# Optimization experiments

Measured on AMD Instinct MI355X. Metric: run time of the kernel, lower is better.

## Reference

```python
import jax, jax.numpy as jnp
import numpy as np

SCALAR_DIM = 452          # 2 + 6 + (110+1)*4
GRID_C, GRID_H, GRID_W = 2, 32, 18
GRID_FLAT = GRID_C * GRID_H * GRID_W  # 1152
OBS_DIM = SCALAR_DIM + GRID_FLAT      # 1604
CNN_OUT, SC_OUT, HID, N_ACT = 128, 64, 128, 2305
CNN_FLAT = 64 * 8 * 5                 # 32x18 -> 16x9 -> 8x5
T, B = 256, 128


def setup_inputs() -> dict:
    key = jax.random.key(0)
    ks = jax.random.split(key, 24)
    p = lambda k, shape: jax.random.normal(k, shape, jnp.float32) * 0.02
    return dict(
        obs_seq=jax.random.uniform(ks[0], (T, B, OBS_DIM), jnp.float32),
        h0=jnp.zeros((1, B, HID), jnp.float32),
        c0=jnp.zeros((1, B, HID), jnp.float32),
        done_mask=jax.random.randint(ks[1], (T, B), 0, 2) > 0,
        conv1_w=p(ks[2], (32, GRID_C, 3, 3)), conv1_b=jnp.zeros((32,), jnp.float32),
        conv2_w=p(ks[3], (64, 32, 3, 3)),     conv2_b=jnp.zeros((64,), jnp.float32),
        conv3_w=p(ks[4], (64, 64, 3, 3)),     conv3_b=jnp.zeros((64,), jnp.float32),
        fc_w=p(ks[5], (CNN_OUT, CNN_FLAT)),   fc_b=jnp.zeros((CNN_OUT,), jnp.float32),
        s1_w=p(ks[6], (64, SCALAR_DIM)),      s1_b=jnp.zeros((64,), jnp.float32),
        s2_w=p(ks[7], (SC_OUT, 64)),          s2_b=jnp.zeros((SC_OUT,), jnp.float32),
        w_ih=p(ks[8], (4 * HID, CNN_OUT + SC_OUT)),
        w_hh=p(ks[9], (4 * HID, HID)),
        b_ih=jnp.zeros((4 * HID,), jnp.float32),
        b_hh=jnp.zeros((4 * HID,), jnp.float32),
        pol_w=p(ks[10], (N_ACT, HID)), pol_b=jnp.zeros((N_ACT,), jnp.float32),
        val_w=p(ks[11], (1, HID)),     val_b=jnp.zeros((1,), jnp.float32),
    )


def _conv(x, w, b, stride):
    y = jax.lax.conv_general_dilated(
        x, w, (stride, stride), ((1, 1), (1, 1)),
        dimension_numbers=("NCHW", "OIHW", "NCHW"))
    return y + b[None, :, None, None]


def reference(obs_seq, h0, c0, done_mask,
              conv1_w, conv1_b, conv2_w, conv2_b, conv3_w, conv3_b,
              fc_w, fc_b, s1_w, s1_b, s2_w, s2_b,
              w_ih, w_hh, b_ih, b_hh, pol_w, pol_b, val_w, val_b):
    Tt, Bb, _ = obs_seq.shape
    flat = obs_seq.reshape(Tt * Bb, -1)
    scalars = flat[:, :SCALAR_DIM]
    grid = flat[:, SCALAR_DIM:SCALAR_DIM + GRID_FLAT].reshape(-1, GRID_C, GRID_H, GRID_W)

    # CNN encoder
    x = jax.nn.relu(_conv(grid, conv1_w, conv1_b, 1))
    x = jax.nn.relu(_conv(x, conv2_w, conv2_b, 2))
    x = jax.nn.relu(_conv(x, conv3_w, conv3_b, 2))
    cnn = jax.nn.relu(x.reshape(x.shape[0], -1) @ fc_w.T + fc_b)

    # scalar MLP
    sc = jax.nn.relu(jax.nn.relu(scalars @ s1_w.T + s1_b) @ s2_w.T + s2_b)

    emb = jnp.concatenate([cnn, sc], axis=-1).reshape(Tt, Bb, -1)  # (T,B,192)

    # episode-reset mask applied BEFORE each step (for t>0, from done[t-1])
    keep = jnp.concatenate(
        [jnp.ones((1, Bb), jnp.float32),
         1.0 - done_mask[:-1].astype(jnp.float32)], axis=0)[..., None]  # (T,B,1)

    def step(carry, inp):
        h, c = carry
        x_t, k_t = inp
        h = h * k_t
        c = c * k_t
        g = x_t @ w_ih.T + h @ w_hh.T + b_ih + b_hh
        i, f, gg, o = jnp.split(g, 4, axis=-1)  # torch gate order i,f,g,o
        c = jax.nn.sigmoid(f) * c + jax.nn.sigmoid(i) * jnp.tanh(gg)
        h = jax.nn.sigmoid(o) * jnp.tanh(c)
        return (h, c), h

    (h_f, c_f), outs = jax.lax.scan(step, (h0[0], c0[0]), (emb, keep))

    logits = outs @ pol_w.T + pol_b   # (T,B,n_actions)
    values = outs @ val_w.T + val_b   # (T,B,1)
    return logits, values, h_f[None], c_f[None]
```

## Files before the change

kernel.cpp:

```cpp
#include <hip/hip_runtime.h>


typedef __attribute__((ext_vector_type(8))) short v8s;
typedef __attribute__((ext_vector_type(4))) float v4f;
typedef __attribute__((ext_vector_type(4))) unsigned int v4u;

#define DEV static __device__ __forceinline__

DEV unsigned int cvtpk(float lo, float hi){
  unsigned int d;
  asm("v_cvt_pk_bf16_f32 %0, %1, %2" : "=v"(d) : "v"(lo), "v"(hi));
  return d;
}
DEV unsigned short f2bf(float x){ return (unsigned short)(cvtpk(x, x) & 0xffffu); }
DEV float bf2f(unsigned short h){ return __uint_as_float(((unsigned int)h) << 16); }
DEV unsigned int pkbf(float a, float b){ return cvtpk(a, b); }
DEV v4f MFMA(v8s a, v8s b, v4f c){ return __builtin_amdgcn_mfma_f32_16x16x32_bf16(a, b, c, 0, 0, 0); }
DEV v4f vzero(){ v4f z = {0.f, 0.f, 0.f, 0.f}; return z; }
DEV float relu(float x){ return x > 0.f ? x : 0.f; }
DEV float sigm(float x){ return 1.0f / (1.0f + __expf(-x)); }
DEV float tanhfast(float x){
  x = fminf(15.0f, fmaxf(-15.0f, x));
  float e = __expf(2.0f * x);
  return (e - 1.0f) / (e + 1.0f);
}
DEV uint2 pack4(v4f a, float4 b){
  return make_uint2(cvtpk(relu(a[0]+b.x), relu(a[1]+b.y)),
                    cvtpk(relu(a[2]+b.z), relu(a[3]+b.w)));
}
union U8S { v4u u4; v8s s8; };

__global__ __launch_bounds__(256) void pack_all(
    const float* __restrict__ c1w, const float* __restrict__ c2w,
    const float* __restrict__ c3w, const float* __restrict__ fcw,
    const float* __restrict__ s1w, const float* __restrict__ s2w,
    const float* __restrict__ wih, const float* __restrict__ whh,
    const float* __restrict__ pw,
    unsigned short* __restrict__ w1p, unsigned short* __restrict__ w2p,
    unsigned short* __restrict__ w3p, unsigned short* __restrict__ fcp,
    unsigned short* __restrict__ s1p, unsigned short* __restrict__ s2p,
    unsigned short* __restrict__ lsp, unsigned short* __restrict__ pop){
  int b = blockIdx.x;
  const float *src, *src2 = nullptr; unsigned short* dst;
  int N, K, KS, CI, mode, rel;
  if      (b < 4)   { src=c1w; dst=w1p; N=32;  K=24;  KS=1;  CI=2;  mode=4; rel=b; }
  else if (b < 76)  { src=c2w; dst=w2p; N=64;  K=288; KS=9;  CI=32; mode=1; rel=b-4; }
  else if (b < 220) { src=c3w; dst=w3p; N=64;  K=576; KS=18; CI=64; mode=1; rel=b-76; }
  else if (b < 1500){ src=fcw; dst=fcp; N=128; K=2560;KS=80; CI=0;  mode=2; rel=b-220; }
  else if (b < 1620){ src=s1w; dst=s1p; N=64;  K=452; KS=15; CI=0;  mode=0; rel=b-1500; }
  else if (b < 1636){ src=s2w; dst=s2p; N=64;  K=64;  KS=2;  CI=0;  mode=0; rel=b-1620; }
  else if (b < 2276){ src=wih; src2=whh; dst=lsp; N=512; K=320; KS=10; CI=0; mode=3; rel=b-1636; }
  else              { src=pw;  dst=pop; N=2305;K=128; KS=4;  CI=0;  mode=0; rel=b-2276; }
  int idx = rel * 256 + threadIdx.x;
  int e  = idx & 7;
  int l  = (idx >> 3) & 63;
  int fs = idx >> 9;
  int ks = fs % KS;
  int nt = fs / KS;
  int n = nt * 16 + (l & 15);
  int k = ks * 32 + (l >> 4) * 8 + e;
  float v = 0.f;
  if (n < N && k < K){
    if (mode == 0)      v = src[n * K + k];
    else if (mode == 1){ int p9 = k / CI, ci = k - p9 * CI; v = src[(n * CI + ci) * 9 + p9]; }
    else if (mode == 2){ int pos = k >> 6, ci = k & 63;     v = src[n * 2560 + ci * 40 + pos]; }
    else if (mode == 3) v = (k < 192) ? src[n * 192 + k] : src2[n * 128 + (k - 192)];
    else { int dy = k >> 3, r = k & 7, dx = r >> 1, ci = r & 1;
           if (dx < 3) v = src[(n * 2 + ci) * 9 + dy * 3 + dx]; }
  }
  dst[idx] = f2bf(v);
}

__global__ __launch_bounds__(512) void bias_kernel(const float* __restrict__ bih,
    const float* __restrict__ bhh, float* __restrict__ bias512){
  int t = threadIdx.x;
  if (t < 512) bias512[t] = bih[t] + bhh[t];
}

__global__ __launch_bounds__(256) void mlp_kernel(const float* __restrict__ obs,
    const unsigned short* __restrict__ s1p, const unsigned short* __restrict__ s2p,
    const float* __restrict__ s1b, const float* __restrict__ s2b,
    unsigned short* __restrict__ emb){
  __shared__ __align__(16) unsigned short xl[32 * 488];
  __shared__ __align__(16) unsigned short h1[32 * 72];
  int tid = threadIdx.x, w = tid >> 6, l = tid & 63, i = l & 15, u = l >> 4;
  long s0 = (long)blockIdx.x * 32;
  for (int idx = tid; idx < 32 * 113; idx += 256){
    int r = idx / 113, q = idx - r * 113;
    float4 v = *(const float4*)&obs[(s0 + r) * 1604 + q * 4];
    *(uint2*)&xl[r * 488 + q * 4] = make_uint2(pkbf(v.x, v.y), pkbf(v.z, v.w));
  }
  for (int idx = tid; idx < 32 * 28; idx += 256){
    int r = idx / 28, k = 452 + (idx - r * 28);
    xl[r * 488 + k] = 0;
  }
  __syncthreads();
  v4f acc0 = vzero(), acc1 = vzero();
  const v8s* F1 = (const v8s*)s1p;
  #pragma unroll
  for (int ks = 0; ks < 15; ++ks){
    v8s bb = F1[(w * 15 + ks) * 64 + l];
    v8s aa0 = *(const v8s*)&xl[(0 * 16 + i) * 488 + ks * 32 + u * 8];
    v8s aa1 = *(const v8s*)&xl[(1 * 16 + i) * 488 + ks * 32 + u * 8];
    acc0 = MFMA(aa0, bb, acc0);
    acc1 = MFMA(aa1, bb, acc1);
  }
  float b1 = s1b[w * 16 + i];
  #pragma unroll
  for (int r = 0; r < 4; ++r){
    float v0 = relu(acc0[r] + b1);
    float v1 = relu(acc1[r] + b1);
    h1[(u * 4 + r) * 72 + w * 16 + i] = f2bf(v0);
    h1[(16 + u * 4 + r) * 72 + w * 16 + i] = f2bf(v1);
  }
  __syncthreads();
  v4f a20 = vzero(), a21 = vzero();
  const v8s* F2 = (const v8s*)s2p;
  #pragma unroll
  for (int ks = 0; ks < 2; ++ks){
    v8s bb = F2[(w * 2 + ks) * 64 + l];
    v8s aa0 = *(const v8s*)&h1[(0 * 16 + i) * 72 + ks * 32 + u * 8];
    v8s aa1 = *(const v8s*)&h1[(1 * 16 + i) * 72 + ks * 32 + u * 8];
    a20 = MFMA(aa0, bb, a20);
    a21 = MFMA(aa1, bb, a21);
  }
  float b2 = s2b[w * 16 + i];
  #pragma unroll
  for (int r = 0; r < 4; ++r){
    float v0 = relu(a20[r] + b2);
    float v1 = relu(a21[r] + b2);
    emb[(s0 + u * 4 + r) * 192 + 128 + w * 16 + i] = f2bf(v0);
    emb[(s0 + 16 + u * 4 + r) * 192 + 128 + w * 16 + i] = f2bf(v1);
  }
}

#define ACT1o 0
#define ACT2o 43520
#define GRIDo 68864
#define SWZ(p) ((((p) >> 1) & 7) << 4)

__global__ __launch_bounds__(512, 2) void conv_kernel(const float* __restrict__ obs,
    const unsigned short* __restrict__ w1p, const unsigned short* __restrict__ w2p,
    const unsigned short* __restrict__ w3p,
    const float* __restrict__ b1v, const float* __restrict__ b2v, const float* __restrict__ b3v,
    unsigned short* __restrict__ act3g){
  __shared__ __align__(16) char lds[74496];
  int tid = threadIdx.x, w = tid >> 6, l = tid & 63, i = l & 15, u = l >> 4;
  int ct = w & 3;
  int ph = w >> 2;
  const v8s* W1 = (const v8s*)w1p;
  const v8s* W2 = (const v8s*)w2p;
  const v8s* W3 = (const v8s*)w3p;
  v8s w1f0 = W1[l], w1f1 = W1[64 + l];
  float4 bc1a = *(const float4*)&b1v[u * 4];
  float4 bc1b = *(const float4*)&b1v[16 + u * 4];
  float4 bc2  = *(const float4*)&b2v[ct * 16 + u * 4];
  float4 bc3  = *(const float4*)&b3v[ct * 16 + u * 4];
  for (int idx = tid; idx < 18624; idx += 512) *(unsigned int*)(lds + idx * 4) = 0u;
  int soff[4];
  #pragma unroll
  for (int j = 0; j < 4; ++j){
    int p = tid * 4 + j, r = p / 18, c = p - r * 18;
    soff[j] = ((r + 1) * 20 + (c + 1)) * 4;
  }
  __syncthreads();
  long sbase = (long)blockIdx.x * 64;
  if (tid < 144){
    const float4* gp = (const float4*)(obs + sbase * 1604 + 452);
    float4 a = gp[tid], b = gp[tid + 144];
    *(unsigned int*)(lds + GRIDo + soff[0]) = pkbf(a.x, b.x);
    *(unsigned int*)(lds + GRIDo + soff[1]) = pkbf(a.y, b.y);
    *(unsigned int*)(lds + GRIDo + soff[2]) = pkbf(a.z, b.z);
    *(unsigned int*)(lds + GRIDo + soff[3]) = pkbf(a.w, b.w);
  }
  __syncthreads();

  int praw3 = ph * 16 + i;
  int oh3 = praw3 / 5, ow3 = praw3 - oh3 * 5;
  int pr3 = (2 * oh3) * 11 + 2 * ow3;
  int praw3s = 32 + i;
  int pos3s = praw3s > 39 ? 39 : praw3s;
  int oh3s = pos3s / 5, ow3s = pos3s - oh3s * 5;
  int pr3s = (2 * oh3s) * 11 + 2 * ow3s;
  bool small3 = (w < 4);

  for (int it = 0; it < 64; ++it){
    long s = sbase + it;
    int gbo = GRIDo + (it & 1) * 2816;
    int z2; asm("s_mov_b32 %0, 0" : "=s"(z2) : "s"(it));
    v8s w2f[9];
    #pragma unroll
    for (int t = 0; t < 9; ++t) w2f[t] = W2[(ct * 9 + t) * 64 + l + z2];
    float4 pa, pb; bool pf = (it < 63) && (tid < 144);
    if (pf){
      const float4* gp = (const float4*)(obs + (s + 1) * 1604 + 452);
      pa = gp[tid]; pb = gp[tid + 144];
    }
    #pragma unroll
    for (int k = 0; k < 5; ++k){
      int ntl = w + 8 * k;
      if (ntl < 36){
        int pos = ntl * 16 + i;
        int oh = pos / 18, ow = pos - oh * 18;
        int glin = gbo + ((oh + u) * 20 + ow) * 4;
        U8S gv;
        gv.u4.x = *(const unsigned int*)(lds + glin);
        gv.u4.y = *(const unsigned int*)(lds + glin + 4);
        gv.u4.z = *(const unsigned int*)(lds + glin + 8);
        gv.u4.w = *(const unsigned int*)(lds + glin + 12);
        v4f a0 = MFMA(w1f0, gv.s8, vzero());
        v4f a1 = MFMA(w1f1, gv.s8, vzero());
        int p1 = (oh + 1) * 20 + (ow + 1);
        int sA = SWZ(p1);
        *(uint2*)(lds + ACT1o + ((p1 * 64 + u * 8) ^ sA))      = pack4(a0, bc1a);
        *(uint2*)(lds + ACT1o + ((p1 * 64 + 32 + u * 8) ^ sA)) = pack4(a1, bc1b);
      }
    }
    __syncthreads();
    #pragma unroll
    for (int kk = 0; kk < 5; ++kk){
      int ntl = ph + 2 * kk;
      if (ntl < 9){
        int pos2 = ntl * 16 + i;
        int oh = pos2 / 9, ow = pos2 - oh * 9;
        int pr0 = (2 * oh) * 20 + 2 * ow;
        v4f a = vzero();
        #pragma unroll
        for (int dy = 0; dy < 3; ++dy)
          #pragma unroll
          for (int dx = 0; dx < 3; ++dx){
            int p = pr0 + dy * 20 + dx;
            int byte = (p * 64 + u * 16) ^ SWZ(p);
            v8s bf = *(const v8s*)(lds + ACT1o + byte);
            a = MFMA(w2f[dy * 3 + dx], bf, a);
          }
        int p2 = (oh + 1) * 11 + (ow + 1);
        *(uint2*)(lds + ACT2o + ((p2 * 128 + ct * 32 + u * 8) ^ SWZ(p2))) = pack4(a, bc2);
      }
    }
    if (pf){
      int gbn = GRIDo + ((it + 1) & 1) * 2816;
      *(unsigned int*)(lds + gbn + soff[0]) = pkbf(pa.x, pb.x);
      *(unsigned int*)(lds + gbn + soff[1]) = pkbf(pa.y, pb.y);
      *(unsigned int*)(lds + gbn + soff[2]) = pkbf(pa.z, pb.z);
      *(unsigned int*)(lds + gbn + soff[3]) = pkbf(pa.w, pb.w);
    }
    __syncthreads();
    {
      int z3; asm("s_mov_b32 %0, 0" : "=s"(z3) : "s"(it));
      v4f c3 = vzero(), c3s = vzero();
      #pragma unroll
      for (int ksh = 0; ksh < 2; ++ksh){
        v8s w3h[9];
        #pragma unroll
        for (int t = 0; t < 9; ++t) w3h[t] = W3[(ct * 18 + ksh * 9 + t) * 64 + l + z3];
        #pragma unroll
        for (int t = 0; t < 9; ++t){
          int ks = ksh * 9 + t, tap = ks >> 1, h = ks & 1;
          int dy = tap / 3, dx = tap - dy * 3;
          int dpp = dy * 11 + dx;
          {
            int p = pr3 + dpp;
            int byte = (p * 128 + h * 64 + u * 16) ^ SWZ(p);
            v8s bf = *(const v8s*)(lds + ACT2o + byte);
            c3 = MFMA(w3h[t], bf, c3);
          }
          if (small3){
            int p = pr3s + dpp;
            int byte = (p * 128 + h * 64 + u * 16) ^ SWZ(p);
            v8s bf = *(const v8s*)(lds + ACT2o + byte);
            c3s = MFMA(w3h[t], bf, c3s);
          }
        }
      }
      unsigned short* dg = act3g + s * 2560;
      *(uint2*)(dg + praw3 * 64 + ct * 16 + u * 4) = pack4(c3, bc3);
      if (small3 && praw3s < 40)
        *(uint2*)(dg + praw3s * 64 + ct * 16 + u * 4) = pack4(c3s, bc3);
    }
  }
}

__global__ __launch_bounds__(256) void fc_kernel(const unsigned short* __restrict__ act3g,
    const unsigned short* __restrict__ fcp, const float* __restrict__ fcb,
    unsigned short* __restrict__ emb){
  __shared__ __align__(16) unsigned short al[64 * 264];
  int tid = threadIdx.x, w = tid >> 6, l = tid & 63, i = l & 15, u = l >> 4;
  long s0 = (long)blockIdx.x * 64;
  v4f acc[4][2];
  #pragma unroll
  for (int mt = 0; mt < 4; ++mt){ acc[mt][0] = vzero(); acc[mt][1] = vzero(); }
  const v8s* F = (const v8s*)fcp;
  for (int kc = 0; kc < 10; ++kc){
    __syncthreads();
    for (int idx = tid; idx < 64 * 32; idx += 256){
      int r = idx >> 5, q = idx & 31;
      *(v8s*)&al[r * 264 + q * 8] = *(const v8s*)&act3g[(s0 + r) * 2560 + kc * 256 + q * 8];
    }
    __syncthreads();
    #pragma unroll
    for (int ksl = 0; ksl < 8; ++ksl){
      v8s b0 = F[((w * 2 + 0) * 80 + kc * 8 + ksl) * 64 + l];
      v8s b1 = F[((w * 2 + 1) * 80 + kc * 8 + ksl) * 64 + l];
      #pragma unroll
      for (int mt = 0; mt < 4; ++mt){
        v8s aa = *(const v8s*)&al[(mt * 16 + i) * 264 + ksl * 32 + u * 8];
        acc[mt][0] = MFMA(aa, b0, acc[mt][0]);
        acc[mt][1] = MFMA(aa, b1, acc[mt][1]);
      }
    }
  }
  float fb0 = fcb[(w * 2) * 16 + i], fb1 = fcb[(w * 2 + 1) * 16 + i];
  #pragma unroll
  for (int mt = 0; mt < 4; ++mt)
    #pragma unroll
    for (int r = 0; r < 4; ++r){
      float v0 = relu(acc[mt][0][r] + fb0);
      float v1 = relu(acc[mt][1][r] + fb1);
      emb[(s0 + mt * 16 + u * 4 + r) * 192 + (w * 2) * 16 + i] = f2bf(v0);
      emb[(s0 + mt * 16 + u * 4 + r) * 192 + (w * 2 + 1) * 16 + i] = f2bf(v1);
    }
}

__global__ __launch_bounds__(256) void segprep_kernel(const void* __restrict__ dmask,
    unsigned int* __restrict__ segs, int4* __restrict__ gtab, int* __restrict__ meta){
  __shared__ int cnt[257], off[257], place[257];
  __shared__ int notInt;
  int tid = threadIdx.x;
  for (int idx = tid; idx < 257; idx += 256){ cnt[idx] = 0; place[idx] = 0; }
  if (tid == 0) notInt = 0;
  __syncthreads();
  const unsigned char* p8 = (const unsigned char*)dmask;
  int nz = 0;
  for (int idx = tid; idx < 2048; idx += 256)
    if (p8[idx * 4 + 1] | p8[idx * 4 + 2] | p8[idx * 4 + 3]) nz = 1;
  if (nz) notInt = 1;
  __syncthreads();
  bool m32 = (notInt == 0);
  const int* p32 = (const int*)dmask;
  if (tid < 128){
    int b = tid, ts = 0;
    for (int t = 0; t < 256; ++t){
      bool d = (t == 255) ? true : (m32 ? (p32[t * 128 + b] != 0) : (p8[t * 128 + b] != 0));
      if (d){ atomicAdd(&cnt[t - ts + 1], 1); ts = t + 1; }
    }
  }
  __syncthreads();
  if (tid == 0){
    int acc = 0;
    for (int len = 1; len <= 256; ++len){ off[len] = acc; acc += cnt[len]; }
    int G = 0;
    for (int len = 1; len <= 256; ++len){
      int c = cnt[len], g = 0;
      while (c > 0){
        int take = c < 32 ? c : 32;
        gtab[G] = make_int4(len, off[len] + g * 32, take, 0);
        ++G; c -= 32; ++g;
      }
    }
    meta[0] = G;
  }
  __syncthreads();
  if (tid < 128){
    int b = tid, ts = 0;
    for (int t = 0; t < 256; ++t){
      bool d = (t == 255) ? true : (m32 ? (p32[t * 128 + b] != 0) : (p8[t * 128 + b] != 0));
      if (d){
        int len = t - ts + 1;
        int slot = off[len] + atomicAdd(&place[len], 1);
        segs[slot] = (unsigned int)(b | (ts << 8));
        ts = t + 1;
      }
    }
  }
}

__global__ __launch_bounds__(512) void lstm_kernel(
    const unsigned short* __restrict__ emb, const unsigned short* __restrict__ lstmp,
    const float* __restrict__ bias512,
    const float* __restrict__ h0, const float* __restrict__ c0,
    const unsigned int* __restrict__ segs, const int4* __restrict__ gtab,
    const int* __restrict__ meta,
    unsigned short* __restrict__ outsb, float* __restrict__ hf, float* __restrict__ cf){
  int grp = blockIdx.x;
  if (grp >= meta[0]) return;
  int4 gd = gtab[grp];
  int len = gd.x, base = gd.y, nseg = gd.z;
  __shared__ __align__(16) unsigned short hbuf[2][32 * 136];
  __shared__ int sb[32], st[32];
  int tid = threadIdx.x, w = tid >> 6, l = tid & 63, i = l & 15, u = l >> 4;
  if (tid < 32){
    unsigned int sv = segs[base + (tid < nseg ? tid : 0)];
    sb[tid] = (int)(sv & 127u);
    st[tid] = (int)((sv >> 8) & 255u);
  }
  __syncthreads();
  int j = w * 16 + i;
  float cst[2][4];
  #pragma unroll
  for (int mt = 0; mt < 2; ++mt)
    #pragma unroll
    for (int r = 0; r < 4; ++r){
      int slot = mt * 16 + u * 4 + r;
      float cv = 0.f, hv = 0.f;
      if (st[slot] == 0){ cv = c0[sb[slot] * 128 + j]; hv = h0[sb[slot] * 128 + j]; }
      cst[mt][r] = cv;
      hbuf[0][slot * 136 + j] = f2bf(hv);
    }
  float bi = bias512[j], bff = bias512[128 + j], bg = bias512[256 + j], bo = bias512[384 + j];
  int bA0 = sb[i], tA0 = st[i];
  int bA1 = sb[16 + i], tA1 = st[16 + i];
  __syncthreads();
  const v8s* LP = (const v8s*)lstmp;
  for (int step = 0; step < len; ++step){
    int pb = step & 1;
    v4f gi0 = vzero(), gi1 = vzero(), gf0 = vzero(), gf1 = vzero();
    v4f gg0 = vzero(), gg1 = vzero(), go0 = vzero(), go1 = vzero();
    #pragma unroll
    for (int ks = 0; ks < 10; ++ks){
      v8s a0, a1;
      if (ks < 6){
        a0 = *(const v8s*)&emb[((long)(tA0 + step) * 128 + bA0) * 192 + ks * 32 + u * 8];
        a1 = *(const v8s*)&emb[((long)(tA1 + step) * 128 + bA1) * 192 + ks * 32 + u * 8];
      } else {
        int koff = (ks - 6) * 32 + u * 8;
        a0 = *(const v8s*)&hbuf[pb][i * 136 + koff];
        a1 = *(const v8s*)&hbuf[pb][(16 + i) * 136 + koff];
      }
      v8s b_i = LP[((w) * 10 + ks) * 64 + l];
      v8s b_f = LP[((w + 8) * 10 + ks) * 64 + l];
      v8s b_g = LP[((w + 16) * 10 + ks) * 64 + l];
      v8s b_o = LP[((w + 24) * 10 + ks) * 64 + l];
      gi0 = MFMA(a0, b_i, gi0); gi1 = MFMA(a1, b_i, gi1);
      gf0 = MFMA(a0, b_f, gf0); gf1 = MFMA(a1, b_f, gf1);
      gg0 = MFMA(a0, b_g, gg0); gg1 = MFMA(a1, b_g, gg1);
      go0 = MFMA(a0, b_o, go0); go1 = MFMA(a1, b_o, go1);
    }
    #pragma unroll
    for (int mt = 0; mt < 2; ++mt)
      #pragma unroll
      for (int r = 0; r < 4; ++r){
        int slot = mt * 16 + u * 4 + r;
        float giv = mt ? gi1[r] : gi0[r];
        float gfv = mt ? gf1[r] : gf0[r];
        float ggv = mt ? gg1[r] : gg0[r];
        float gov = mt ? go1[r] : go0[r];
        float iv = sigm(giv + bi);
        float fv = sigm(gfv + bff);
        float gv = tanhfast(ggv + bg);
        float ov = sigm(gov + bo);
        float cv = fv * cst[mt][r] + iv * gv;
        cst[mt][r] = cv;
        float hv = ov * tanhfast(cv);
        unsigned short hb = f2bf(hv);
        hbuf[pb ^ 1][slot * 136 + j] = hb;
        if (slot < nseg){
          outsb[((long)(st[slot] + step) * 128 + sb[slot]) * 128 + j] = hb;
          if (st[slot] + len == 256 && step == len - 1){
            hf[sb[slot] * 128 + j] = hv;
            cf[sb[slot] * 128 + j] = cv;
          }
        }
      }
    __syncthreads();
  }
}

__global__ __launch_bounds__(256) void heads_kernel(const unsigned short* __restrict__ outsb,
    const unsigned short* __restrict__ polp, const float* __restrict__ polb,
    const float* __restrict__ vw, const float* __restrict__ vb,
    float* __restrict__ logits, float* __restrict__ values){
  __shared__ __align__(16) unsigned short al[64 * 136];
  int tid = threadIdx.x, w = tid >> 6, l = tid & 63, i = l & 15, u = l >> 4;
  long s0 = (long)blockIdx.x * 64;
  for (int idx = tid; idx < 64 * 16; idx += 256){
    int r = idx >> 4, q = idx & 15;
    *(v8s*)&al[r * 136 + q * 8] = *(const v8s*)&outsb[(s0 + r) * 128 + q * 8];
  }
  __syncthreads();
  v8s af[4][4];
  #pragma unroll
  for (int mt = 0; mt < 4; ++mt)
    #pragma unroll
    for (int ks = 0; ks < 4; ++ks)
      af[mt][ks] = *(const v8s*)&al[(mt * 16 + i) * 136 + ks * 32 + u * 8];
  const v8s* P = (const v8s*)polp;
  for (int nt = w; nt < 145; nt += 4){
    v4f acc[4];
    #pragma unroll
    for (int mt = 0; mt < 4; ++mt) acc[mt] = vzero();
    #pragma unroll
    for (int ks = 0; ks < 4; ++ks){
      v8s bb = P[(nt * 4 + ks) * 64 + l];
      #pragma unroll
      for (int mt = 0; mt < 4; ++mt) acc[mt] = MFMA(af[mt][ks], bb, acc[mt]);
    }
    int n = nt * 16 + i;
    if (n < 2305){
      float pbv = polb[n];
      #pragma unroll
      for (int mt = 0; mt < 4; ++mt)
        #pragma unroll
        for (int r = 0; r < 4; ++r)
          logits[(s0 + mt * 16 + u * 4 + r) * 2305 + n] = acc[mt][r] + pbv;
    }
  }
  float vacc = 0.f;
  #pragma unroll
  for (int g = 0; g < 4; ++g){
    float4 vA = *(const float4*)&vw[g * 32 + u * 8];
    float4 vB = *(const float4*)&vw[g * 32 + u * 8 + 4];
    v8s xv = *(const v8s*)&al[(w * 16 + i) * 136 + g * 32 + u * 8];
    vacc += bf2f((unsigned short)xv[0]) * vA.x + bf2f((unsigned short)xv[1]) * vA.y
          + bf2f((unsigned short)xv[2]) * vA.z + bf2f((unsigned short)xv[3]) * vA.w
          + bf2f((unsigned short)xv[4]) * vB.x + bf2f((unsigned short)xv[5]) * vB.y
          + bf2f((unsigned short)xv[6]) * vB.z + bf2f((unsigned short)xv[7]) * vB.w;
  }
  vacc += __shfl_xor(vacc, 16);
  vacc += __shfl_xor(vacc, 32);
  if (u == 0) values[s0 + w * 16 + i] = vacc + vb[0];
}

extern "C" void kernel_launch(void* const* d_in, const int* in_sizes, int n_in,
                              void* d_out, int out_size, void* d_ws, size_t ws_size,
                              hipStream_t stream){
  (void)in_sizes; (void)n_in; (void)out_size; (void)ws_size;
  const float* obs = (const float*)d_in[0];
  const float* h0  = (const float*)d_in[1];
  const float* c0  = (const float*)d_in[2];
  const void*  dm  = d_in[3];
  const float* c1w = (const float*)d_in[4];  const float* c1b = (const float*)d_in[5];
  const float* c2w = (const float*)d_in[6];  const float* c2b = (const float*)d_in[7];
  const float* c3w = (const float*)d_in[8];  const float* c3b = (const float*)d_in[9];
  const float* fcw = (const float*)d_in[10]; const float* fcb = (const float*)d_in[11];
  const float* s1w = (const float*)d_in[12]; const float* s1b = (const float*)d_in[13];
  const float* s2w = (const float*)d_in[14]; const float* s2b = (const float*)d_in[15];
  const float* wih = (const float*)d_in[16]; const float* whh = (const float*)d_in[17];
  const float* bih = (const float*)d_in[18]; const float* bhh = (const float*)d_in[19];
  const float* pw  = (const float*)d_in[20]; const float* pb  = (const float*)d_in[21];
  const float* vw  = (const float*)d_in[22]; const float* vb  = (const float*)d_in[23];

  char* ws = (char*)d_ws;
  size_t off = 0;
  auto take = [&](size_t sz)->char*{
    char* p = ws + off; off = (off + sz + 255) & ~(size_t)255; return p;
  };
  unsigned short* emb    = (unsigned short*)take(32768UL * 192 * 2);
  unsigned short* outsb  = (unsigned short*)take(32768UL * 128 * 2);
  unsigned short* w1p    = (unsigned short*)take(1024UL * 2);
  unsigned short* w2p    = (unsigned short*)take(18432UL * 2);
  unsigned short* w3p    = (unsigned short*)take(36864UL * 2);
  unsigned short* fcp    = (unsigned short*)take(327680UL * 2);
  unsigned short* s1p    = (unsigned short*)take(30720UL * 2);
  unsigned short* s2p    = (unsigned short*)take(4096UL * 2);
  unsigned short* lsp    = (unsigned short*)take(163840UL * 2);
  unsigned short* pop    = (unsigned short*)take(296960UL * 2);
  float*          b512   = (float*)take(512UL * 4);
  unsigned int*   segs   = (unsigned int*)take(32768UL * 4);
  int4*           gtab   = (int4*)take(1280UL * 16);
  int*            meta   = (int*)take(256);

  float* outp   = (float*)d_out;
  float* logits = outp;
  float* values = outp + 75530240L;
  float* hf     = outp + 75563008L;
  float* cf     = outp + 75579392L;
  unsigned short* act3g = (unsigned short*)d_out;

  dim3 b256(256), b512t(512);
  pack_all<<<dim3(3436), b256, 0, stream>>>(c1w, c2w, c3w, fcw, s1w, s2w, wih, whh, pw,
                                            w1p, w2p, w3p, fcp, s1p, s2p, lsp, pop);
  bias_kernel<<<dim3(1), b512t, 0, stream>>>(bih, bhh, b512);
  segprep_kernel<<<dim3(1), b256, 0, stream>>>(dm, segs, gtab, meta);
  mlp_kernel<<<dim3(1024), b256, 0, stream>>>(obs, s1p, s2p, s1b, s2b, emb);
  conv_kernel<<<dim3(512), b512t, 0, stream>>>(obs, w1p, w2p, w3p, c1b, c2b, c3b, act3g);
  fc_kernel<<<dim3(512), b256, 0, stream>>>(act3g, fcp, fcb, emb);
  lstm_kernel<<<dim3(1280), b512t, 0, stream>>>(emb, lsp, b512, h0, c0, segs, gtab, meta,
                                                outsb, hf, cf);
  heads_kernel<<<dim3(512), b256, 0, stream>>>(outsb, pop, pb, vw, vb, logits, values);
}
```

Before: 1.172 ms.

## Cut conv kernel register pressure and raise launch-bounds occupancy target

Result: slower. 1.968 ms (+67.9%).

```diff
diff --git a/kernel.cpp b/kernel.cpp
--- a/kernel.cpp
+++ b/kernel.cpp
@@ -139,7 +139,7 @@
 #define GRIDo 68864
 #define SWZ(p) ((((p) >> 1) & 7) << 4)
 
-__global__ __launch_bounds__(512, 2) void conv_kernel(const float* __restrict__ obs,
+__global__ __launch_bounds__(512, 4) void conv_kernel(const float* __restrict__ obs,
     const unsigned short* __restrict__ w1p, const unsigned short* __restrict__ w2p,
     const unsigned short* __restrict__ w3p,
     const float* __restrict__ b1v, const float* __restrict__ b2v, const float* __restrict__ b3v,
@@ -175,6 +175,17 @@
   }
   __syncthreads();
 
+  int pr2k[5], wo2k[5];
+  #pragma unroll
+  for (int kk = 0; kk < 5; ++kk){
+    int ntl = ph + 2 * kk;
+    int ntc = ntl < 9 ? ntl : 0;
+    int pos2 = ntc * 16 + i;
+    int oh = pos2 / 9, ow = pos2 - oh * 9;
+    pr2k[kk] = (2 * oh) * 20 + 2 * ow;
+    int p2 = (oh + 1) * 11 + (ow + 1);
+    wo2k[kk] = ACT2o + ((p2 * 128 + ct * 32 + u * 8) ^ SWZ(p2));
+  }
   int praw3 = ph * 16 + i;
   int oh3 = praw3 / 5, ow3 = praw3 - oh3 * 5;
   int pr3 = (2 * oh3) * 11 + 2 * ow3;
@@ -187,10 +198,6 @@
   for (int it = 0; it < 64; ++it){
     long s = sbase + it;
     int gbo = GRIDo + (it & 1) * 2816;
-    int z2; asm("s_mov_b32 %0, 0" : "=s"(z2) : "s"(it));
-    v8s w2f[9];
-    #pragma unroll
-    for (int t = 0; t < 9; ++t) w2f[t] = W2[(ct * 9 + t) * 64 + l + z2];
     float4 pa, pb; bool pf = (it < 63) && (tid < 144);
     if (pf){
       const float4* gp = (const float4*)(obs + (s + 1) * 1604 + 452);
@@ -216,28 +223,6 @@
         *(uint2*)(lds + ACT1o + ((p1 * 64 + 32 + u * 8) ^ sA)) = pack4(a1, bc1b);
       }
     }
-    __syncthreads();
-    #pragma unroll
-    for (int kk = 0; kk < 5; ++kk){
-      int ntl = ph + 2 * kk;
-      if (ntl < 9){
-        int pos2 = ntl * 16 + i;
-        int oh = pos2 / 9, ow = pos2 - oh * 9;
-        int pr0 = (2 * oh) * 20 + 2 * ow;
-        v4f a = vzero();
-        #pragma unroll
-        for (int dy = 0; dy < 3; ++dy)
-          #pragma unroll
-          for (int dx = 0; dx < 3; ++dx){
-            int p = pr0 + dy * 20 + dx;
-            int byte = (p * 64 + u * 16) ^ SWZ(p);
-            v8s bf = *(const v8s*)(lds + ACT1o + byte);
-            a = MFMA(w2f[dy * 3 + dx], bf, a);
-          }
-        int p2 = (oh + 1) * 11 + (ow + 1);
-        *(uint2*)(lds + ACT2o + ((p2 * 128 + ct * 32 + u * 8) ^ SWZ(p2))) = pack4(a, bc2);
-      }
-    }
     if (pf){
       int gbn = GRIDo + ((it + 1) & 1) * 2816;
       *(unsigned int*)(lds + gbn + soff[0]) = pkbf(pa.x, pb.x);
@@ -247,29 +232,59 @@
     }
     __syncthreads();
     {
+      int z2; asm("s_mov_b32 %0, 0" : "=s"(z2) : "s"(it));
+      v4f a2[5];
+      #pragma unroll
+      for (int kk = 0; kk < 5; ++kk) a2[kk] = vzero();
+      #pragma unroll
+      for (int tc = 0; tc < 3; ++tc){
+        v8s wc0 = W2[(ct * 9 + tc * 3 + 0) * 64 + l + z2];
+        v8s wc1 = W2[(ct * 9 + tc * 3 + 1) * 64 + l + z2];
+        v8s wc2 = W2[(ct * 9 + tc * 3 + 2) * 64 + l + z2];
+        #pragma unroll
+        for (int kk = 0; kk < 5; ++kk){
+          if (ph + 2 * kk < 9){
+            int pb0 = pr2k[kk] + tc * 20;
+            #pragma unroll
+            for (int dx = 0; dx < 3; ++dx){
+              int p = pb0 + dx;
+              int byte = (p * 64 + u * 16) ^ SWZ(p);
+              v8s bf = *(const v8s*)(lds + ACT1o + byte);
+              a2[kk] = MFMA(dx == 0 ? wc0 : (dx == 1 ? wc1 : wc2), bf, a2[kk]);
+            }
+          }
+        }
+      }
+      #pragma unroll
+      for (int kk = 0; kk < 5; ++kk)
+        if (ph + 2 * kk < 9) *(uint2*)(lds + wo2k[kk]) = pack4(a2[kk], bc2);
+    }
+    __syncthreads();
+    {
       int z3; asm("s_mov_b32 %0, 0" : "=s"(z3) : "s"(it));
       v4f c3 = vzero(), c3s = vzero();
       #pragma unroll
-      for (int ksh = 0; ksh < 2; ++ksh){
-        v8s w3h[9];
+      for (int tc = 0; tc < 6; ++tc){
+        v8s wc0 = W3[(ct * 18 + tc * 3 + 0) * 64 + l + z3];
+        v8s wc1 = W3[(ct * 18 + tc * 3 + 1) * 64 + l + z3];
+        v8s wc2 = W3[(ct * 18 + tc * 3 + 2) * 64 + l + z3];
         #pragma unroll
-        for (int t = 0; t < 9; ++t) w3h[t] = W3[(ct * 18 + ksh * 9 + t) * 64 + l + z3];
-        #pragma unroll
-        for (int t = 0; t < 9; ++t){
-          int ks = ksh * 9 + t, tap = ks >> 1, h = ks & 1;
+        for (int j = 0; j < 3; ++j){
+          int ks = tc * 3 + j, tap = ks >> 1, h = ks & 1;
           int dy = tap / 3, dx = tap - dy * 3;
           int dpp = dy * 11 + dx;
+          v8s wcj = j == 0 ? wc0 : (j == 1 ? wc1 : wc2);
           {
             int p = pr3 + dpp;
             int byte = (p * 128 + h * 64 + u * 16) ^ SWZ(p);
             v8s bf = *(const v8s*)(lds + ACT2o + byte);
-            c3 = MFMA(w3h[t], bf, c3);
+            c3 = MFMA(wcj, bf, c3);
           }
           if (small3){
             int p = pr3s + dpp;
             int byte = (p * 128 + h * 64 + u * 16) ^ SWZ(p);
             v8s bf = *(const v8s*)(lds + ACT2o + byte);
-            c3s = MFMA(w3h[t], bf, c3s);
+            c3s = MFMA(wcj, bf, c3s);
           }
         }
       }
```
